# Kernel optimization log

Measured on AMD Instinct MI355X. Metric: run time of the kernel, lower is better.

Reference implementation:

```python
import jax, jax.numpy as jnp
import numpy as np

H = 1024
N_HEADS = 16
HEAD = H // N_HEADS
EPS = 1e-5


def setup_inputs() -> dict:
    key = jax.random.key(0)
    ks = jax.random.split(key, 12)
    B, T = 4, 2048
    s = 1.0 / np.sqrt(H)
    return {
        "x": jax.random.normal(ks[0], (B, T, H), dtype=jnp.float32),
        "attention_mask": jax.random.randint(ks[1], (B, T), 0, 2) == 1,
        "ln_g": jnp.ones((H,), jnp.float32),
        "ln_b": jnp.zeros((H,), jnp.float32),
        "wq": jax.random.normal(ks[2], (H, H), jnp.float32) * s,
        "bq": jnp.zeros((H,), jnp.float32),
        "wk": jax.random.normal(ks[3], (H, H), jnp.float32) * s,
        "bk": jnp.zeros((H,), jnp.float32),
        "wv": jax.random.normal(ks[4], (H, H), jnp.float32) * s,
        "bv": jnp.zeros((H,), jnp.float32),
        "wo": jax.random.normal(ks[5], (H, H), jnp.float32) * s,
        "bo": jnp.zeros((H,), jnp.float32),
    }


def _heads(t, B, T):
    # (B,T,H) -> (B,n,T,h)
    return t.reshape(B, T, N_HEADS, HEAD).transpose(0, 2, 1, 3)


def reference(x, attention_mask, ln_g, ln_b, wq, bq, wk, bk, wv, bv, wo, bo):
    B, T, _ = x.shape
    # LayerNorm
    mu = jnp.mean(x, axis=-1, keepdims=True)
    var = jnp.mean(jnp.square(x - mu), axis=-1, keepdims=True)
    h = (x - mu) * jax.lax.rsqrt(var + EPS) * ln_g + ln_b
    # QKV projections (torch Linear: y = x @ W.T + b)
    q = _heads(h @ wq.T + bq, B, T)
    k = _heads(h @ wk.T + bk, B, T)
    v = _heads(h @ wv.T + bv, B, T)
    # scores (B,n,T,T)
    scores = jnp.einsum('bnqh,bnkh->bnqk', q, k) / np.sqrt(HEAD).astype(np.float32)
    scores = jnp.where(attention_mask[:, None, None, :], -jnp.inf, scores)
    probs = jax.nn.softmax(scores, axis=-1)
    # dropout prob = 0.0 -> identity
    c = jnp.einsum('bnqk,bnkh->bnqh', probs, v)
    c = c.transpose(0, 2, 1, 3).reshape(B, T, H)
    return x + (c @ wo.T + bo)
```

## Files before the change

### kernel.cpp

```cpp
#include <hip/hip_runtime.h>
#include <hip/hip_bf16.h>

typedef short short8 __attribute__((ext_vector_type(8)));
typedef float f32x4 __attribute__((ext_vector_type(4)));
typedef float f32x16 __attribute__((ext_vector_type(16)));

#define HDIM 1024
#define TSEQ 2048
#define BATCH 4
#define NH 16
#define HD 64
#define SCALE_Q 0.18033688011f
#define BHT (BATCH * NH * TSEQ)

__device__ __forceinline__ unsigned short f2bf(float f) {
  union { float f; unsigned u; } x; x.f = f;
  unsigned r = x.u + 0x7fffu + ((x.u >> 16) & 1u);
  return (unsigned short)(r >> 16);
}

__device__ __forceinline__ float bf2f(unsigned short u) {
  union { unsigned u; float f; } z; z.u = (unsigned)u << 16; return z.f;
}

__device__ __forceinline__ unsigned pk2(float a, float b) {
  __hip_bfloat162 h2 = __float22bfloat162_rn(float2{a, b});
  union { __hip_bfloat162 h; unsigned u; } u2; u2.h = h2;
  return u2.u;
}

__device__ __forceinline__ int swz(int row, int slot) { return slot ^ (row & 7); }

typedef const __attribute__((address_space(1))) void* gas_ptr;
typedef __attribute__((address_space(3))) void* las_ptr;
__device__ __forceinline__ void gl2lds16(const void* g, void* l) {
  __builtin_amdgcn_global_load_lds((gas_ptr)g, (las_ptr)l, 16, 0, 0);
}

__device__ __forceinline__ void pswap(unsigned& x, unsigned& y) {
#if __has_builtin(__builtin_amdgcn_permlane32_swap)
  typedef int i32x2 __attribute__((ext_vector_type(2)));
  i32x2 r = __builtin_amdgcn_permlane32_swap((int)x, (int)y, false, false);
  x = (unsigned)r[0]; y = (unsigned)r[1];
#else
  unsigned px = (unsigned)__shfl_xor((int)x, 32);
  unsigned py = (unsigned)__shfl_xor((int)y, 32);
  bool hiHalf = (threadIdx.x & 32) != 0;
  unsigned nx = hiHalf ? py : x;
  unsigned ny = hiHalf ? y : px;
  x = nx; y = ny;
#endif
}

__global__ __launch_bounds__(256) void convert_w(
    const float* __restrict__ wq, const float* __restrict__ wk,
    const float* __restrict__ wv, const float* __restrict__ wo,
    unsigned short* __restrict__ out) {
  size_t i = ((size_t)blockIdx.x * 256 + threadIdx.x) * 4;
  int which = (int)(i >> 20);
  const float* src = which == 0 ? wq : which == 1 ? wk : which == 2 ? wv : wo;
  size_t off = i & ((1u << 20) - 1);
  float4 v = *reinterpret_cast<const float4*>(src + off);
  unsigned lo = (unsigned)f2bf(v.x) | ((unsigned)f2bf(v.y) << 16);
  unsigned hi = (unsigned)f2bf(v.z) | ((unsigned)f2bf(v.w) << 16);
  uint2 o; o.x = lo; o.y = hi;
  *reinterpret_cast<uint2*>(out + i) = o;
}

__global__ __launch_bounds__(256) void compact_mask(
    const int* __restrict__ mask, int* __restrict__ idx,
    float* __restrict__ bias, int* __restrict__ meta) {
  const int b = blockIdx.x, tid = threadIdx.x;
  const int l = tid & 63, w = tid >> 6;
  const int* mp = mask + b * TSEQ;
  const int base = tid * 8;
  int keep[8]; int cnt = 0;
#pragma unroll
  for (int j = 0; j < 8; ++j) { keep[j] = (mp[base + j] == 0); cnt += keep[j]; }
  int inc = cnt;
  for (int s = 1; s < 64; s <<= 1) {
    int t = __shfl_up(inc, s);
    if (l >= s) inc += t;
  }
  __shared__ int wsum[4];
  if (l == 63) wsum[w] = inc;
  __syncthreads();
  int wbase = 0;
#pragma unroll
  for (int i = 0; i < 4; ++i) if (i < w) wbase += wsum[i];
  const int total = wsum[0] + wsum[1] + wsum[2] + wsum[3];
  int pos = wbase + inc - cnt;
#pragma unroll
  for (int j = 0; j < 8; ++j)
    if (keep[j]) idx[b * TSEQ + (pos++)] = base + j;
  for (int i = tid; i < TSEQ; i += 256) {
    if (i >= total) idx[b * TSEQ + i] = 0;
    bias[b * TSEQ + i] = (i < total) ? -16.0f : -1e30f;
  }
  if (tid == 0) {
    int cntp = (total + 63) & ~63;
    if (cntp == 0) cntp = 64;
    meta[b * 2 + 0] = cntp;
    meta[b * 2 + 1] = cntp >> 6;
  }
}

__global__ __launch_bounds__(256) void ln_kernel(
    const float* __restrict__ x, const float* __restrict__ g,
    const float* __restrict__ bta, unsigned short* __restrict__ h) {
  int row = blockIdx.x;
  int tid = threadIdx.x;
  const float* xr = x + (size_t)row * HDIM;
  float4 v = *reinterpret_cast<const float4*>(xr + tid * 4);
  float s = v.x + v.y + v.z + v.w;
  float sq = v.x * v.x + v.y * v.y + v.z * v.z + v.w * v.w;
  for (int m = 32; m; m >>= 1) { s += __shfl_xor(s, m); sq += __shfl_xor(sq, m); }
  __shared__ float red[8];
  int w = tid >> 6, l = tid & 63;
  if (l == 0) { red[w] = s; red[4 + w] = sq; }
  __syncthreads();
  s = red[0] + red[1] + red[2] + red[3];
  sq = red[4] + red[5] + red[6] + red[7];
  float mu = s * (1.0f / HDIM);
  float var = sq * (1.0f / HDIM) - mu * mu;
  float inv = rsqrtf(var + 1e-5f);
  float4 gv = *reinterpret_cast<const float4*>(g + tid * 4);
  float4 bv = *reinterpret_cast<const float4*>(bta + tid * 4);
  unsigned short o0 = f2bf((v.x - mu) * inv * gv.x + bv.x);
  unsigned short o1 = f2bf((v.y - mu) * inv * gv.y + bv.y);
  unsigned short o2 = f2bf((v.z - mu) * inv * gv.z + bv.z);
  unsigned short o3 = f2bf((v.w - mu) * inv * gv.w + bv.w);
  uint2 o; o.x = (unsigned)o0 | ((unsigned)o1 << 16); o.y = (unsigned)o2 | ((unsigned)o3 << 16);
  *reinterpret_cast<uint2*>(h + (size_t)row * HDIM + tid * 4) = o;
}

template <int MODE>
__global__ __launch_bounds__(512) void gemm_k(
    const unsigned short* __restrict__ A, const unsigned short* __restrict__ Wb,
    const float* __restrict__ b0, const float* __restrict__ b1, const float* __restrict__ b2,
    unsigned short* __restrict__ o0, unsigned short* __restrict__ o1, unsigned short* __restrict__ o2,
    const float* __restrict__ xres, float* __restrict__ outf,
    const int* __restrict__ idxp, const int* __restrict__ metap) {
  __shared__ __align__(16) unsigned short Alds[128 * 64];
  __shared__ __align__(16) unsigned short Wlds[128 * 64];
  const int flat = blockIdx.x;
  const int xcd = flat & 7, g = flat >> 3;
  const int bm = (g & 7) * 8 + xcd;
  const int bn = g >> 3;
  const int z = (MODE == 0) ? (bn >> 3) : 0;
  if (MODE == 0 && z != 0) {
    int bb = bm >> 4, t0 = (bm & 15) * 128;
    if (t0 >= metap[bb * 2]) return;
  }
  const float* bias = (z == 0) ? b0 : (z == 1) ? b1 : b2;
  unsigned short* obf = (z == 0) ? o0 : (z == 1) ? o1 : o2;
  const int tid = threadIdx.x;
  const int l = tid & 63, w = tid >> 6;
  const int wr = (w >> 2) * 64, wc = (w & 3) * 32;
  const int lrow = l & 15, lk = l >> 4;
  const int sr = l >> 3;
  const int sslot = (l & 7) ^ (sr & 7);
  int agrow[2];
#pragma unroll
  for (int p = 0; p < 2; ++p) {
    int grow = bm * 128 + w * 16 + p * 8 + sr;
    if (MODE == 0 && z != 0) {
      int bb = grow >> 11;
      agrow[p] = bb * TSEQ + idxp[grow];
    } else agrow[p] = grow;
  }
  f32x4 acc[4][2] = {};
  for (int kt = 0; kt < 16; ++kt) {
    __syncthreads();
#pragma unroll
    for (int p = 0; p < 2; ++p) {
      int rb = w * 16 + p * 8;
      gl2lds16(A + (size_t)agrow[p] * HDIM + kt * 64 + sslot * 8, Alds + rb * 64);
      gl2lds16(Wb + (size_t)(bn * 128 + rb + sr) * HDIM + kt * 64 + sslot * 8, Wlds + rb * 64);
    }
    __syncthreads();
#pragma unroll
    for (int ks = 0; ks < 2; ++ks) {
      short8 af[4], bfr[2];
#pragma unroll
      for (int rt = 0; rt < 4; ++rt) {
        int row = wr + rt * 16 + lrow;
        af[rt] = *reinterpret_cast<const short8*>(reinterpret_cast<char*>(Alds) + row * 128 + swz(row, ks * 4 + lk) * 16);
      }
#pragma unroll
      for (int ct = 0; ct < 2; ++ct) {
        int row = wc + ct * 16 + lrow;
        bfr[ct] = *reinterpret_cast<const short8*>(reinterpret_cast<char*>(Wlds) + row * 128 + swz(row, ks * 4 + lk) * 16);
      }
#pragma unroll
      for (int rt = 0; rt < 4; ++rt)
#pragma unroll
        for (int ct = 0; ct < 2; ++ct)
          acc[rt][ct] = __builtin_amdgcn_mfma_f32_16x16x32_bf16(af[rt], bfr[ct], acc[rt][ct], 0, 0, 0);
    }
  }
#pragma unroll
  for (int rt = 0; rt < 4; ++rt) {
#pragma unroll
    for (int ct = 0; ct < 2; ++ct) {
      int ncol = bn * 128 + wc + ct * 16 + lrow;
      int col = ncol & (HDIM - 1);
      float bv = bias[col];
      if (MODE == 0 && z == 2) {
        int mrow0 = bm * 128 + wr + rt * 16 + lk * 4;
        int bb = mrow0 >> 11, t0 = mrow0 & (TSEQ - 1);
        int head = (col >> 6) & 15, d = col & 63;
        uint2 pw;
        pw.x = pk2(acc[rt][ct][0] + bv, acc[rt][ct][1] + bv);
        pw.y = pk2(acc[rt][ct][2] + bv, acc[rt][ct][3] + bv);
        *reinterpret_cast<uint2*>(obf + ((size_t)(bb * NH + head) * HD + d) * TSEQ + t0) = pw;
      } else {
#pragma unroll
        for (int r = 0; r < 4; ++r) {
          int mrow = bm * 128 + wr + rt * 16 + lk * 4 + r;
          float val = acc[rt][ct][r] + bv;
          if (MODE == 0) {
            if (z == 0) val *= SCALE_Q;
            int bb = mrow >> 11, t = mrow & (TSEQ - 1);
            int head = (col >> 6) & 15, d = col & 63;
            obf[((size_t)(bb * NH + head) * TSEQ + t) * HD + d] = f2bf(val);
          } else {
            size_t idx = (size_t)mrow * HDIM + col;
            outf[idx] = val + xres[idx];
          }
        }
      }
    }
  }
}

__global__ __launch_bounds__(512) void attn_kernel(
    const unsigned short* __restrict__ q_s, const unsigned short* __restrict__ k_s,
    const unsigned short* __restrict__ vt_s, const float* __restrict__ mzf,
    const int* __restrict__ meta, float* __restrict__ pl,
    unsigned short* __restrict__ pa) {
  __shared__ __align__(16) unsigned short Klds[2][64 * 64];
  __shared__ __align__(16) unsigned short Vlds[2][64 * 64];
  const int flat = blockIdx.x & 511;
  const int split = blockIdx.x >> 9;
  const int qb = (flat >> 3) & 7;
  const int hb = ((flat >> 6) << 3) | (flat & 7);
  const int head = hb & 15, b = hb >> 4;
  const int ntiles = meta[b * 2 + 1];
  const int nt0 = (ntiles + 1) >> 1;
  const int tb = split ? nt0 : 0;
  const int te = split ? ntiles : nt0;
  const unsigned short* qp = q_s + ((size_t)(b * NH + head) * TSEQ + qb * 256) * HD;
  const unsigned short* kp = k_s + (size_t)(b * NH + head) * TSEQ * HD;
  const unsigned short* vtp = vt_s + (size_t)(b * NH + head) * HD * TSEQ;
  const float* mp = mzf + b * TSEQ;
  const int tid = threadIdx.x, l = tid & 63, w = tid >> 6;
  const int ln = l & 31, h = l >> 5;
  const int sr = l >> 3;
  const int sslot = (l & 7) ^ (sr & 7);

  short8 qf[4];
  {
    const unsigned short* qrp = qp + (size_t)(w * 32 + ln) * HD;
#pragma unroll
    for (int dk = 0; dk < 4; ++dk)
      qf[dk] = *reinterpret_cast<const short8*>(qrp + dk * 16 + h * 8);
  }

  f32x16 acc0 = {}, acc1 = {};
  float lsum = 0.0f;

  auto KSTAGE = [&](int kv2, int bi2) {
    int rb = w * 8;
    gl2lds16(kp + (size_t)(kv2 * 64 + rb + sr) * HD + sslot * 8, &Klds[bi2][rb * 64]);
  };
  auto VSTAGE = [&](int kv2, int bi2) {
    int rb = w * 8;
    gl2lds16(vtp + (size_t)(rb + sr) * TSEQ + kv2 * 64 + sslot * 8, &Vlds[bi2][rb * 64]);
  };

  if (tb < te) { KSTAGE(tb, 0); VSTAGE(tb, 0); }

  for (int kv = tb; kv < te; ++kv) {
    const int bi = (kv - tb) & 1;
    const char* Kb = reinterpret_cast<const char*>(&Klds[bi][0]);
    const char* Vb = reinterpret_cast<const char*>(&Vlds[bi][0]);
    __syncthreads();
    if (kv + 1 < te) { KSTAGE(kv + 1, bi ^ 1); VSTAGE(kv + 1, bi ^ 1); }

    f32x16 st0, st1;
    if (kv == ntiles - 1) {
#pragma unroll
      for (int kt2 = 0; kt2 < 2; ++kt2) {
        f32x16& s = kt2 ? st1 : st0;
#pragma unroll
        for (int g = 0; g < 4; ++g) {
          f32x4 m4 = *reinterpret_cast<const f32x4*>(mp + kv * 64 + kt2 * 32 + g * 8 + 4 * h);
#pragma unroll
          for (int t = 0; t < 4; ++t) s[g * 4 + t] = m4[t];
        }
      }
    } else {
#pragma unroll
      for (int r = 0; r < 16; ++r) { st0[r] = -16.0f; st1[r] = -16.0f; }
    }

    __builtin_amdgcn_s_setprio(1);
#pragma unroll
    for (int kt2 = 0; kt2 < 2; ++kt2) {
      f32x16& s = kt2 ? st1 : st0;
      int row = kt2 * 32 + ln;
#pragma unroll
      for (int dk = 0; dk < 4; ++dk) {
        int slot = (dk * 2 + h) ^ (row & 7);
        short8 kf = *reinterpret_cast<const short8*>(Kb + row * 128 + slot * 16);
        s = __builtin_amdgcn_mfma_f32_32x32x16_bf16(kf, qf[dk], s, 0, 0, 0);
      }
    }
    __builtin_amdgcn_s_setprio(0);

#pragma unroll
    for (int r = 0; r < 16; ++r) {
      st0[r] = __builtin_amdgcn_exp2f(st0[r]);
      st1[r] = __builtin_amdgcn_exp2f(st1[r]);
    }
    {
      f32x16 sv = st0 + st1;
      float s0 = (sv[0] + sv[1]) + (sv[2] + sv[3]);
      float s1 = (sv[4] + sv[5]) + (sv[6] + sv[7]);
      float s2 = (sv[8] + sv[9]) + (sv[10] + sv[11]);
      float s3 = (sv[12] + sv[13]) + (sv[14] + sv[15]);
      lsum += (s0 + s1) + (s2 + s3);
    }

    __builtin_amdgcn_s_setprio(1);
#pragma unroll
    for (int ks = 0; ks < 4; ++ks) {
      const f32x16& p2 = (ks >> 1) ? st1 : st0;
      const int a = 8 * (ks & 1);
      unsigned X0 = pk2(p2[a + 0], p2[a + 1]);
      unsigned X1 = pk2(p2[a + 2], p2[a + 3]);
      unsigned Y0 = pk2(p2[a + 4], p2[a + 5]);
      unsigned Y1 = pk2(p2[a + 6], p2[a + 7]);
      pswap(X0, Y0);
      pswap(X1, Y1);
      union { unsigned u[4]; short8 s; } pf;
      pf.u[0] = X0; pf.u[1] = X1; pf.u[2] = Y0; pf.u[3] = Y1;
#pragma unroll
      for (int dc = 0; dc < 2; ++dc) {
        int row = dc * 32 + ln;
        int slot = (ks * 2 + h) ^ (row & 7);
        short8 vf = *reinterpret_cast<const short8*>(Vb + row * 128 + slot * 16);
        if (dc == 0)
          acc0 = __builtin_amdgcn_mfma_f32_32x32x16_bf16(pf.s, vf, acc0, 0, 0, 0);
        else
          acc1 = __builtin_amdgcn_mfma_f32_32x32x16_bf16(pf.s, vf, acc1, 0, 0, 0);
      }
    }
    __builtin_amdgcn_s_setprio(0);
  }

  lsum += __shfl_xor(lsum, 32);
  const size_t rowbase = (size_t)(b * NH + head) * TSEQ + qb * 256 + w * 32;
  if (l < 32) pl[(size_t)split * BHT + rowbase + l] = lsum;
  unsigned short* pap = pa + (size_t)split * BHT * HD + rowbase * HD;
#pragma unroll
  for (int r = 0; r < 16; ++r) {
    int cr = (r & 3) + 8 * (r >> 2) + 4 * h;
    pap[cr * HD + ln] = f2bf(acc0[r]);
    pap[cr * HD + 32 + ln] = f2bf(acc1[r]);
  }
}

__global__ __launch_bounds__(256) void combine_k(
    const unsigned short* __restrict__ pa, const float* __restrict__ pl,
    unsigned short* __restrict__ c) {
  int gid = blockIdx.x * 256 + threadIdx.x;
  int row = gid >> 3;
  int d0 = (gid & 7) << 3;
  float inv = 1.0f / (pl[row] + pl[BHT + row]);
  const unsigned short* a0 = pa + (size_t)row * HD + d0;
  const unsigned short* a1 = a0 + (size_t)BHT * HD;
  short8 v0 = *reinterpret_cast<const short8*>(a0);
  short8 v1 = *reinterpret_cast<const short8*>(a1);
  union { unsigned short u[8]; short8 s; } o;
#pragma unroll
  for (int j = 0; j < 8; ++j)
    o.u[j] = f2bf((bf2f((unsigned short)v0[j]) + bf2f((unsigned short)v1[j])) * inv);
  int bh = row >> 11, t = row & (TSEQ - 1);
  int b = bh >> 4, head = bh & 15;
  *reinterpret_cast<short8*>(c + ((size_t)(b * TSEQ + t)) * HDIM + head * HD + d0) = o.s;
}

extern "C" void kernel_launch(void* const* d_in, const int* in_sizes, int n_in,
                              void* d_out, int out_size, void* d_ws, size_t ws_size,
                              hipStream_t stream) {
  const float* x   = (const float*)d_in[0];
  const int* mask  = (const int*)d_in[1];
  const float* lng = (const float*)d_in[2];
  const float* lnb = (const float*)d_in[3];
  const float* wq  = (const float*)d_in[4];
  const float* bq  = (const float*)d_in[5];
  const float* wk  = (const float*)d_in[6];
  const float* bk  = (const float*)d_in[7];
  const float* wv  = (const float*)d_in[8];
  const float* bv  = (const float*)d_in[9];
  const float* wo  = (const float*)d_in[10];
  const float* bo  = (const float*)d_in[11];
  float* out = (float*)d_out;
  char* ws = (char*)d_ws;

  unsigned short* h   = (unsigned short*)ws;
  unsigned short* wbf = (unsigned short*)(ws + (16u << 20));
  unsigned short* qs  = (unsigned short*)(ws + (24u << 20));
  unsigned short* ksb = (unsigned short*)(ws + (40u << 20));
  unsigned short* vt  = (unsigned short*)(ws + (56u << 20));
  float*          mzf = (float*)(ws + (72u << 20));
  int*            idx = (int*)(ws + (72u << 20) + (64u << 10));
  int*            met = (int*)(ws + (72u << 20) + (128u << 10));
  unsigned short* pa  = (unsigned short*)(ws + (76u << 20));
  float*          pl  = (float*)(ws + (108u << 20));
  unsigned short* c   = h;

  convert_w<<<4096, 256, 0, stream>>>(wq, wk, wv, wo, wbf);
  compact_mask<<<BATCH, 256, 0, stream>>>(mask, idx, mzf, met);
  ln_kernel<<<BATCH * TSEQ, 256, 0, stream>>>(x, lng, lnb, h);
  gemm_k<0><<<dim3(1536), 512, 0, stream>>>(h, wbf, bq, bk, bv, qs, ksb, vt,
                                            nullptr, nullptr, idx, met);
  attn_kernel<<<dim3(1024), dim3(512), 0, stream>>>(qs, ksb, vt, mzf, met, pl, pa);
  combine_k<<<dim3(BHT * HD / 8 / 256), 256, 0, stream>>>(pa, pl, c);
  gemm_k<1><<<dim3(512), 512, 0, stream>>>(c, wbf + (size_t)3 * HDIM * HDIM, bo, nullptr, nullptr,
                                           nullptr, nullptr, nullptr, x, out, nullptr, nullptr);
}
```

Before: 155.5 us.

## Fuse split-attention combine into output projection GEMM A-tile loading

Removes the separate combine kernel and instead has the output-projection GEMM read both attention split partials and their row sums directly, normalizing and converting to bf16 while writing its A tile into LDS. The next k-tile's partials are prefetched into registers to overlap with compute. This drops a kernel launch and the round trip of the combined context tensor through global memory. In exchange, each GEMM block redoes the combine for its rows across all 8 column blocks, so partial loads are repeated and the A path moves from async global-to-LDS loads to register loads plus a VALU combine.

```diff
diff --git a/kernel.cpp b/kernel.cpp
--- a/kernel.cpp
+++ b/kernel.cpp
@@ -140,7 +140,8 @@
     const float* __restrict__ b0, const float* __restrict__ b1, const float* __restrict__ b2,
     unsigned short* __restrict__ o0, unsigned short* __restrict__ o1, unsigned short* __restrict__ o2,
     const float* __restrict__ xres, float* __restrict__ outf,
-    const int* __restrict__ idxp, const int* __restrict__ metap) {
+    const int* __restrict__ idxp, const int* __restrict__ metap,
+    const unsigned short* __restrict__ pa01, const float* __restrict__ pl01) {
   __shared__ __align__(16) unsigned short Alds[128 * 64];
   __shared__ __align__(16) unsigned short Wlds[128 * 64];
   const int flat = blockIdx.x;
@@ -160,6 +161,7 @@
   const int lrow = l & 15, lk = l >> 4;
   const int sr = l >> 3;
   const int sslot = (l & 7) ^ (sr & 7);
+
   int agrow[2];
 #pragma unroll
   for (int p = 0; p < 2; ++p) {
@@ -169,14 +171,58 @@
       agrow[p] = bb * TSEQ + idxp[grow];
     } else agrow[p] = grow;
   }
+
+  int crow[2]; size_t pbase[2];
+  short8 rv0[2], rv1[2]; float rls[2];
+  if (MODE == 1) {
+#pragma unroll
+    for (int cc = 0; cc < 2; ++cc) {
+      int chunk = tid + cc * 512;
+      crow[cc] = chunk >> 3;
+      int mrow = bm * 128 + crow[cc];
+      int b_ = mrow >> 11, t_ = mrow & (TSEQ - 1);
+      pbase[cc] = (size_t)(b_ * NH) * TSEQ + t_;
+    }
+  }
+  auto LOADA1 = [&](int kt) {
+#pragma unroll
+    for (int cc = 0; cc < 2; ++cc) {
+      int s = (tid + cc * 512) & 7;
+      size_t prow = pbase[cc] + (size_t)kt * TSEQ;
+      rls[cc] = pl01[prow] + pl01[BHT + prow];
+      const unsigned short* a0 = pa01 + prow * HD + s * 8;
+      rv0[cc] = *reinterpret_cast<const short8*>(a0);
+      rv1[cc] = *reinterpret_cast<const short8*>(a0 + (size_t)BHT * HD);
+    }
+  };
+  auto WRITEA1 = [&]() {
+#pragma unroll
+    for (int cc = 0; cc < 2; ++cc) {
+      int s = (tid + cc * 512) & 7, r = crow[cc];
+      float inv = 1.0f / rls[cc];
+      union { unsigned u[4]; short8 s8; } o;
+#pragma unroll
+      for (int j = 0; j < 4; ++j)
+        o.u[j] = pk2((bf2f((unsigned short)rv0[cc][2 * j]) + bf2f((unsigned short)rv1[cc][2 * j])) * inv,
+                     (bf2f((unsigned short)rv0[cc][2 * j + 1]) + bf2f((unsigned short)rv1[cc][2 * j + 1])) * inv);
+      *reinterpret_cast<short8*>(reinterpret_cast<char*>(Alds) + r * 128 + swz(r, s) * 16) = o.s8;
+    }
+  };
+
+  if (MODE == 1) LOADA1(0);
   f32x4 acc[4][2] = {};
   for (int kt = 0; kt < 16; ++kt) {
     __syncthreads();
 #pragma unroll
     for (int p = 0; p < 2; ++p) {
       int rb = w * 16 + p * 8;
-      gl2lds16(A + (size_t)agrow[p] * HDIM + kt * 64 + sslot * 8, Alds + rb * 64);
       gl2lds16(Wb + (size_t)(bn * 128 + rb + sr) * HDIM + kt * 64 + sslot * 8, Wlds + rb * 64);
+      if (MODE == 0)
+        gl2lds16(A + (size_t)agrow[p] * HDIM + kt * 64 + sslot * 8, Alds + rb * 64);
+    }
+    if (MODE == 1) {
+      WRITEA1();
+      if (kt + 1 < 16) LOADA1(kt + 1);
     }
     __syncthreads();
 #pragma unroll
@@ -372,26 +418,6 @@
   }
 }
 
-__global__ __launch_bounds__(256) void combine_k(
-    const unsigned short* __restrict__ pa, const float* __restrict__ pl,
-    unsigned short* __restrict__ c) {
-  int gid = blockIdx.x * 256 + threadIdx.x;
-  int row = gid >> 3;
-  int d0 = (gid & 7) << 3;
-  float inv = 1.0f / (pl[row] + pl[BHT + row]);
-  const unsigned short* a0 = pa + (size_t)row * HD + d0;
-  const unsigned short* a1 = a0 + (size_t)BHT * HD;
-  short8 v0 = *reinterpret_cast<const short8*>(a0);
-  short8 v1 = *reinterpret_cast<const short8*>(a1);
-  union { unsigned short u[8]; short8 s; } o;
-#pragma unroll
-  for (int j = 0; j < 8; ++j)
-    o.u[j] = f2bf((bf2f((unsigned short)v0[j]) + bf2f((unsigned short)v1[j])) * inv);
-  int bh = row >> 11, t = row & (TSEQ - 1);
-  int b = bh >> 4, head = bh & 15;
-  *reinterpret_cast<short8*>(c + ((size_t)(b * TSEQ + t)) * HDIM + head * HD + d0) = o.s;
-}
-
 extern "C" void kernel_launch(void* const* d_in, const int* in_sizes, int n_in,
                               void* d_out, int out_size, void* d_ws, size_t ws_size,
                               hipStream_t stream) {
@@ -420,15 +446,13 @@
   int*            met = (int*)(ws + (72u << 20) + (128u << 10));
   unsigned short* pa  = (unsigned short*)(ws + (76u << 20));
   float*          pl  = (float*)(ws + (108u << 20));
-  unsigned short* c   = h;
 
   convert_w<<<4096, 256, 0, stream>>>(wq, wk, wv, wo, wbf);
   compact_mask<<<BATCH, 256, 0, stream>>>(mask, idx, mzf, met);
   ln_kernel<<<BATCH * TSEQ, 256, 0, stream>>>(x, lng, lnb, h);
   gemm_k<0><<<dim3(1536), 512, 0, stream>>>(h, wbf, bq, bk, bv, qs, ksb, vt,
-                                            nullptr, nullptr, idx, met);
+                                            nullptr, nullptr, idx, met, nullptr, nullptr);
   attn_kernel<<<dim3(1024), dim3(512), 0, stream>>>(qs, ksb, vt, mzf, met, pl, pa);
-  combine_k<<<dim3(BHT * HD / 8 / 256), 256, 0, stream>>>(pa, pl, c);
-  gemm_k<1><<<dim3(512), 512, 0, stream>>>(c, wbf + (size_t)3 * HDIM * HDIM, bo, nullptr, nullptr,
-                                           nullptr, nullptr, nullptr, x, out, nullptr, nullptr);
-}
+  gemm_k<1><<<dim3(512), 512, 0, stream>>>(nullptr, wbf + (size_t)3 * HDIM * HDIM, bo, nullptr, nullptr,
+                                           nullptr, nullptr, nullptr, x, out, nullptr, nullptr, pa, pl);
+}
```

Measured after the change: 158.8 us. 2.1% more time.
